# Kernel optimization log

Measured on AMD Instinct MI355X. Metric: run time of the kernel, lower is better.

Reference implementation:

```python
import jax, jax.numpy as jnp
import numpy as np

B, H, W, C = 16, 64, 64, 512
C2 = C // 2
LN_EPS = 1e-3  # Keras LayerNormalization default epsilon


def setup_inputs() -> dict:
    key = jax.random.key(0)
    ks = jax.random.split(key, 8)
    s = 0.02
    return {
        "x": jax.random.normal(ks[0], (B, H, W, C), dtype=jnp.float32),
        "ch_wv_w": jax.random.normal(ks[1], (C, C2), dtype=jnp.float32) * s,
        "ch_wv_b": jnp.zeros((C2,), jnp.float32),
        "ch_wq_w": jax.random.normal(ks[2], (C, 1), dtype=jnp.float32) * s,
        "ch_wq_b": jnp.zeros((1,), jnp.float32),
        "ch_wz_w": jax.random.normal(ks[3], (C2, C), dtype=jnp.float32) * s,
        "ch_wz_b": jnp.zeros((C,), jnp.float32),
        "ln_gamma": jnp.ones((C,), jnp.float32),
        "ln_beta": jnp.zeros((C,), jnp.float32),
        "sp_wv_w": jax.random.normal(ks[4], (C, C2), dtype=jnp.float32) * s,
        "sp_wv_b": jnp.zeros((C2,), jnp.float32),
        "sp_wq_w": jax.random.normal(ks[5], (C, C2), dtype=jnp.float32) * s,
        "sp_wq_b": jnp.zeros((C2,), jnp.float32),
    }


def reference(x, ch_wv_w, ch_wv_b, ch_wq_w, ch_wq_b, ch_wz_w, ch_wz_b,
              ln_gamma, ln_beta, sp_wv_w, sp_wv_b, sp_wq_w, sp_wq_b):
    b, h, w, c = x.shape
    n = h * w
    c2 = c // 2

    # ---- channel-only branch ----
    # 1x1 convs are pointwise GEMMs over the channel dim
    ch_wv = jnp.einsum('bhwc,cd->bhwd', x, ch_wv_w) + ch_wv_b      # (B,H,W,C/2)
    ch_wq = jnp.einsum('bhwc,co->bhwo', x, ch_wq_w) + ch_wq_b      # (B,H,W,1)
    ch_wv = ch_wv.reshape(b, n, c2)                                # (B,N,C/2)
    ch_wq = jax.nn.softmax(ch_wq.reshape(b, n, 1), axis=1)         # softmax over N
    ch_wz = jnp.einsum('bnd,bno->bd', ch_wv, ch_wq)                # (B,C/2)
    ch_wz = jnp.einsum('bd,dc->bc', ch_wz, ch_wz_w) + ch_wz_b      # (B,C)

    # LayerNorm over axes [1,2,3] of (B,1,1,C) == normalize over C
    mean = jnp.mean(ch_wz, axis=-1, keepdims=True)
    var = jnp.var(ch_wz, axis=-1, keepdims=True)
    ch_wz = (ch_wz - mean) * jax.lax.rsqrt(var + LN_EPS) * ln_gamma + ln_beta
    channel_weight = jax.nn.sigmoid(ch_wz)[:, None, None, :]       # (B,1,1,C)
    channel_out = channel_weight * x                               # (B,H,W,C)

    # ---- spatial-only branch ----
    sp_wv = jnp.einsum('bhwc,cd->bhwd', channel_out, sp_wv_w) + sp_wv_b  # (B,H,W,C/2)
    sp_wq = jnp.einsum('bhwc,cd->bhwd', channel_out, sp_wq_w) + sp_wq_b  # (B,H,W,C/2)
    sp_wq = jnp.mean(sp_wq, axis=(1, 2))                           # GAP -> (B,C/2)
    sp_wq = jax.nn.softmax(sp_wq, axis=-1)                         # softmax over C/2
    sp_wv = sp_wv.reshape(b, n, c2)                                # (B,N,C/2)
    sp_wz = jnp.einsum('bd,bnd->bn', sp_wq, sp_wv)                 # (B,N)
    spatial_weight = jax.nn.sigmoid(sp_wz).reshape(b, h, w, 1)     # (B,H,W,1)
    return spatial_weight * channel_out
```

## Files before the change

### kernel.cpp

```cpp
#include <hip/hip_runtime.h>
#include <math.h>

#define BB 16
#define NN 4096
#define CC 512
#define C2 256
#define CHUNKS 64
#define RPC (NN/CHUNKS)
#define NW (CC*C2)

typedef float  f4v __attribute__((ext_vector_type(4)));
typedef unsigned short ushort;
typedef unsigned int   uint;

__device__ __forceinline__ float sigmoidf_(float z){ return 1.0f/(1.0f + __expf(-z)); }
__device__ __forceinline__ float dot8_(float4 a0, float4 a1, float4 b0, float4 b1){
    return a0.x*b0.x + a0.y*b0.y + a0.z*b0.z + a0.w*b0.w
         + a1.x*b1.x + a1.y*b1.y + a1.z*b1.z + a1.w*b1.w;
}
__device__ __forceinline__ ushort f2bf(float f){
    uint u = __float_as_uint(f);
    return (ushort)((u + 0x7FFFu + ((u >> 16) & 1u)) >> 16);
}
__device__ __forceinline__ float2 bfpair(uint v){
    return make_float2(__uint_as_float(v << 16), __uint_as_float(v & 0xFFFF0000u));
}

__global__ __launch_bounds__(256) void k_stats(const float* __restrict__ x,
        const float* __restrict__ wq,
        const float* __restrict__ Wv, const float* __restrict__ Wz,
        const float* __restrict__ Wq2, const float* __restrict__ Wv2,
        float* __restrict__ part_w, float* __restrict__ part_g,
        float* __restrict__ part_d, ushort* __restrict__ wbf)
{
    const int t = threadIdx.x, lane = t & 63, wv = t >> 6;

    if (blockIdx.x >= BB*CHUNKS) {
        const int idx = blockIdx.x - BB*CHUNKS;
        const int mat = idx >> 4;
        const float* src = (mat == 0) ? Wv : (mat == 1) ? Wz : (mat == 2) ? Wq2 : Wv2;
        const int boff = (idx & 15) * 8192;
        ushort* dst = wbf + (long)mat*NW + boff;
        const float* s = src + boff;
        #pragma unroll 8
        for (int e = 0; e < 32; ++e)
            dst[t + e*256] = f2bf(s[t + e*256]);
        return;
    }

    const int b = blockIdx.x / CHUNKS;
    const int k = blockIdx.x % CHUNKS;
    __shared__ float rw[4][CC];
    __shared__ float rg[4][CC];
    __shared__ float rd[4];
    const long base = ((long)b*NN + (long)k*RPC) * CC;

    float4 w0 = *(const float4*)(wq + lane*4);
    float4 w1 = *(const float4*)(wq + 256 + lane*4);
    float4 aw0={0,0,0,0}, aw1={0,0,0,0}, ag0={0,0,0,0}, ag1={0,0,0,0};
    float den = 0.f;

    for (int i = 0; i < RPC/8; ++i) {
        const int r0 = wv*(RPC/4) + 2*i;
        const float* xr0 = x + base + (long)r0*CC;
        const float* xr1 = xr0 + CC;
        float4 a0 = *(const float4*)(xr0 + lane*4);
        float4 a1 = *(const float4*)(xr0 + 256 + lane*4);
        float4 b0 = *(const float4*)(xr1 + lane*4);
        float4 b1 = *(const float4*)(xr1 + 256 + lane*4);
        float da = dot8_(a0, a1, w0, w1);
        float db = dot8_(b0, b1, w0, w1);
        #pragma unroll
        for (int off = 32; off; off >>= 1) {
            da += __shfl_xor(da, off);
            db += __shfl_xor(db, off);
        }
        const float ea = __expf(da);
        const float eb = __expf(db);
        den += ea + eb;
        aw0.x = fmaf(ea,a0.x,fmaf(eb,b0.x,aw0.x)); aw0.y = fmaf(ea,a0.y,fmaf(eb,b0.y,aw0.y));
        aw0.z = fmaf(ea,a0.z,fmaf(eb,b0.z,aw0.z)); aw0.w = fmaf(ea,a0.w,fmaf(eb,b0.w,aw0.w));
        aw1.x = fmaf(ea,a1.x,fmaf(eb,b1.x,aw1.x)); aw1.y = fmaf(ea,a1.y,fmaf(eb,b1.y,aw1.y));
        aw1.z = fmaf(ea,a1.z,fmaf(eb,b1.z,aw1.z)); aw1.w = fmaf(ea,a1.w,fmaf(eb,b1.w,aw1.w));
        ag0.x += a0.x+b0.x; ag0.y += a0.y+b0.y; ag0.z += a0.z+b0.z; ag0.w += a0.w+b0.w;
        ag1.x += a1.x+b1.x; ag1.y += a1.y+b1.y; ag1.z += a1.z+b1.z; ag1.w += a1.w+b1.w;
    }
    *(float4*)&rw[wv][lane*4]     = aw0;
    *(float4*)&rw[wv][256+lane*4] = aw1;
    *(float4*)&rg[wv][lane*4]     = ag0;
    *(float4*)&rg[wv][256+lane*4] = ag1;
    if (lane == 0) rd[wv] = den;
    __syncthreads();

    const long o = (long)(b*CHUNKS + k)*CC;
    part_w[o + t]       = rw[0][t]+rw[1][t]+rw[2][t]+rw[3][t];
    part_w[o + t + 256] = rw[0][t+256]+rw[1][t+256]+rw[2][t+256]+rw[3][t+256];
    part_g[o + t]       = rg[0][t]+rg[1][t]+rg[2][t]+rg[3][t];
    part_g[o + t + 256] = rg[0][t+256]+rg[1][t+256]+rg[2][t+256]+rg[3][t+256];
    if (t == 0) part_d[b*CHUNKS + k] = rd[0]+rd[1]+rd[2]+rd[3];
}

__global__ __launch_bounds__(512) void k_chain(
    const float* __restrict__ part_w, const float* __restrict__ part_g,
    const float* __restrict__ part_d,
    const ushort* __restrict__ wbf,
    const float* __restrict__ bv,  const float* __restrict__ bz,
    const float* __restrict__ lng, const float* __restrict__ lnb,
    const float* __restrict__ bq,  const float* __restrict__ bv2,
    float* __restrict__ cw, float* __restrict__ veff, float* __restrict__ constb)
{
    const int b = blockIdx.x, t = threadIdx.x, lane = t & 63, w = t >> 6;
    const ushort* Wvb  = wbf;
    const ushort* Wzb  = wbf + NW;
    const ushort* Wqb  = wbf + 2*NW;
    const ushort* Wv2b = wbf + 3*NW;
    __shared__ float s_a[CC];
    __shared__ float s_b[CC];
    __shared__ float s_c[CC];
    __shared__ float s_m[C2];
    __shared__ float s_g1[1024];
    __shared__ float s_r[16];

    {
        const float* pwp = part_w + (long)b*CHUNKS*CC + t;
        const float* pgp = part_g + (long)b*CHUNKS*CC + t;
        float pw = 0.f, pg = 0.f;
        #pragma unroll 8
        for (int k = 0; k < CHUNKS; ++k) {
            pw += __builtin_nontemporal_load(pwp + (long)k*CC);
            pg += __builtin_nontemporal_load(pgp + (long)k*CC);
        }
        const float* pd = part_d + b*CHUNKS;
        float den = 0.f;
        #pragma unroll 8
        for (int k = 0; k < CHUNKS; ++k) den += pd[k];
        s_a[t] = pw / den;
        s_b[t] = pg;
    }
    __syncthreads();

    {
        const int pr = t & 127, cq = t >> 7;
        const ushort* wp = Wvb + (long)(cq*128)*C2 + 2*pr;
        const float* xp = s_a + cq*128;
        float ax=0, ay=0, bx=0, by=0;
        #pragma unroll 8
        for (int c = 0; c < 128; c += 2) {
            uint u0 = *(const uint*)(wp + (long)(c  )*C2);
            uint u1 = *(const uint*)(wp + (long)(c+1)*C2);
            float2 p0 = bfpair(u0), p1 = bfpair(u1);
            ax = fmaf(xp[c],   p0.x, ax); ay = fmaf(xp[c],   p0.y, ay);
            bx = fmaf(xp[c+1], p1.x, bx); by = fmaf(xp[c+1], p1.y, by);
        }
        s_g1[cq*256 + pr*2]     = ax + bx;
        s_g1[cq*256 + pr*2 + 1] = ay + by;
    }
    __syncthreads();
    if (t < 256) s_m[t] = s_g1[t] + s_g1[256+t] + s_g1[512+t] + s_g1[768+t] + bv[t];
    __syncthreads();

    {
        const int cp = t & 255, dh = t >> 8;
        const ushort* wp = Wzb + (long)(dh*128)*CC + 2*cp;
        const float* mp = s_m + dh*128;
        float ax=0, ay=0, bx=0, by=0;
        #pragma unroll 8
        for (int d = 0; d < 128; d += 2) {
            uint u0 = *(const uint*)(wp + (long)(d  )*CC);
            uint u1 = *(const uint*)(wp + (long)(d+1)*CC);
            float2 p0 = bfpair(u0), p1 = bfpair(u1);
            ax = fmaf(mp[d],   p0.x, ax); ay = fmaf(mp[d],   p0.y, ay);
            bx = fmaf(mp[d+1], p1.x, bx); by = fmaf(mp[d+1], p1.y, by);
        }
        s_g1[dh*512 + cp*2]     = ax + bx;
        s_g1[dh*512 + cp*2 + 1] = ay + by;
    }
    __syncthreads();
    float zt = s_g1[t] + s_g1[512 + t] + bz[t];

    {
        float sum = zt, sq = zt*zt;
        #pragma unroll
        for (int off = 32; off; off >>= 1) { sum += __shfl_xor(sum, off); sq += __shfl_xor(sq, off); }
        if (lane == 0) { s_r[w] = sum; s_r[8+w] = sq; }
        __syncthreads();
        sum = 0.f; sq = 0.f;
        #pragma unroll
        for (int i = 0; i < 8; ++i) { sum += s_r[i]; sq += s_r[8+i]; }
        const float mean = sum * (1.f/CC);
        const float var  = sq  * (1.f/CC) - mean*mean;
        const float rstd = rsqrtf(var + 1e-3f);
        const float cwt = sigmoidf_((zt - mean)*rstd*lng[t] + lnb[t]);
        cw[b*CC + t] = cwt;
        __syncthreads();
        s_c[t] = cwt;
        s_a[t] = cwt * s_b[t] * (1.f/NN);
    }
    __syncthreads();

    {
        const int pr = t & 127, cq = t >> 7;
        const ushort* wp = Wqb + (long)(cq*128)*C2 + 2*pr;
        const float* xp = s_a + cq*128;
        float ax=0, ay=0, bx=0, by=0;
        #pragma unroll 8
        for (int c = 0; c < 128; c += 2) {
            uint u0 = *(const uint*)(wp + (long)(c  )*C2);
            uint u1 = *(const uint*)(wp + (long)(c+1)*C2);
            float2 p0 = bfpair(u0), p1 = bfpair(u1);
            ax = fmaf(xp[c],   p0.x, ax); ay = fmaf(xp[c],   p0.y, ay);
            bx = fmaf(xp[c+1], p1.x, bx); by = fmaf(xp[c+1], p1.y, by);
        }
        s_g1[cq*256 + pr*2]     = ax + bx;
        s_g1[cq*256 + pr*2 + 1] = ay + by;
    }
    __syncthreads();

    float qv = 0.f;
    if (t < 256) qv = s_g1[t] + s_g1[256+t] + s_g1[512+t] + s_g1[768+t] + bq[t];
    {
        float mx = (t < 256) ? qv : -3.4e38f;
        #pragma unroll
        for (int off = 32; off; off >>= 1) mx = fmaxf(mx, __shfl_xor(mx, off));
        if (lane == 0) s_r[w] = mx;
        __syncthreads();
        mx = s_r[0];
        #pragma unroll
        for (int i = 1; i < 8; ++i) mx = fmaxf(mx, s_r[i]);
        float e = (t < 256) ? __expf(qv - mx) : 0.f;
        float se = e;
        #pragma unroll
        for (int off = 32; off; off >>= 1) se += __shfl_xor(se, off);
        __syncthreads();
        if (lane == 0) s_r[8+w] = se;
        __syncthreads();
        se = 0.f;
        #pragma unroll
        for (int i = 0; i < 8; ++i) se += s_r[8+i];
        const float qn = e / se;
        float cb = (t < 256) ? qn * bv2[t] : 0.f;
        #pragma unroll
        for (int off = 32; off; off >>= 1) cb += __shfl_xor(cb, off);
        if (lane == 0) s_r[w] = cb;
        __syncthreads();
        if (t < 256) s_b[t] = qn;
        if (t == 0) {
            float c_ = 0.f;
            #pragma unroll
            for (int i = 0; i < 8; ++i) c_ += s_r[i];
            constb[b] = c_;
        }
    }
    __syncthreads();

    {
        const int sub = lane & 15;
        float4 q0 = *(const float4*)(s_b + sub*16 + 0);
        float4 q1 = *(const float4*)(s_b + sub*16 + 4);
        float4 q2 = *(const float4*)(s_b + sub*16 + 8);
        float4 q3 = *(const float4*)(s_b + sub*16 + 12);
        for (int it = 0; it < 16; ++it) {
            const int c = (it*8 + w)*4 + (lane >> 4);
            const uint4* wr = (const uint4*)(Wv2b + (long)c*C2) + sub*2;
            uint4 u0 = wr[0], u1 = wr[1];
            float2 p;
            float d = 0.f;
            p = bfpair(u0.x); d += p.x*q0.x + p.y*q0.y;
            p = bfpair(u0.y); d += p.x*q0.z + p.y*q0.w;
            p = bfpair(u0.z); d += p.x*q1.x + p.y*q1.y;
            p = bfpair(u0.w); d += p.x*q1.z + p.y*q1.w;
            p = bfpair(u1.x); d += p.x*q2.x + p.y*q2.y;
            p = bfpair(u1.y); d += p.x*q2.z + p.y*q2.w;
            p = bfpair(u1.z); d += p.x*q3.x + p.y*q3.y;
            p = bfpair(u1.w); d += p.x*q3.z + p.y*q3.w;
            #pragma unroll
            for (int off = 8; off; off >>= 1) d += __shfl_xor(d, off);
            if (sub == 0) veff[b*CC + c] = s_c[c] * d;
        }
    }
}

__global__ __launch_bounds__(256) void k_final(const float* __restrict__ x,
        const float* __restrict__ cw, const float* __restrict__ veff,
        const float* __restrict__ constb, float* __restrict__ out)
{
    const int lane = threadIdx.x & 63;
    const int wv   = threadIdx.x >> 6;
    const long row0 = (long)blockIdx.x * 8 + wv*2;
    const int b = (int)(row0 >> 12);
    const float* vb = veff + b*CC;
    float4 v0 = *(const float4*)(vb + lane*4);
    float4 v1 = *(const float4*)(vb + 256 + lane*4);
    const float* cb = cw + b*CC;
    float4 c0 = *(const float4*)(cb + lane*4);
    float4 c1 = *(const float4*)(cb + 256 + lane*4);
    const float* xr0 = x + row0 * CC;
    float4 a0 = *(const float4*)(xr0 + lane*4);
    float4 a1 = *(const float4*)(xr0 + 256 + lane*4);
    float4 b0 = *(const float4*)(xr0 + CC + lane*4);
    float4 b1 = *(const float4*)(xr0 + CC + 256 + lane*4);
    float d0 = dot8_(a0, a1, v0, v1);
    float d1 = dot8_(b0, b1, v0, v1);
    #pragma unroll
    for (int off = 32; off; off >>= 1) {
        d0 += __shfl_xor(d0, off);
        d1 += __shfl_xor(d1, off);
    }
    const float cbb = constb[b];
    const float sw0 = sigmoidf_(d0 + cbb);
    const float sw1 = sigmoidf_(d1 + cbb);
    f4v o0 = { sw0*c0.x*a0.x, sw0*c0.y*a0.y, sw0*c0.z*a0.z, sw0*c0.w*a0.w };
    f4v o1 = { sw0*c1.x*a1.x, sw0*c1.y*a1.y, sw0*c1.z*a1.z, sw0*c1.w*a1.w };
    f4v o2 = { sw1*c0.x*b0.x, sw1*c0.y*b0.y, sw1*c0.z*b0.z, sw1*c0.w*b0.w };
    f4v o3 = { sw1*c1.x*b1.x, sw1*c1.y*b1.y, sw1*c1.z*b1.z, sw1*c1.w*b1.w };
    __builtin_nontemporal_store(o0, (f4v*)(out + row0*CC + lane*4));
    __builtin_nontemporal_store(o1, (f4v*)(out + row0*CC + 256 + lane*4));
    __builtin_nontemporal_store(o2, (f4v*)(out + row0*CC + CC + lane*4));
    __builtin_nontemporal_store(o3, (f4v*)(out + row0*CC + CC + 256 + lane*4));
}

extern "C" void kernel_launch(void* const* d_in, const int* in_sizes, int n_in,
                              void* d_out, int out_size, void* d_ws, size_t ws_size,
                              hipStream_t stream)
{
    const float* x       = (const float*)d_in[0];
    const float* ch_wv_w = (const float*)d_in[1];
    const float* ch_wv_b = (const float*)d_in[2];
    const float* ch_wq_w = (const float*)d_in[3];
    const float* ch_wz_w = (const float*)d_in[5];
    const float* ch_wz_b = (const float*)d_in[6];
    const float* ln_g    = (const float*)d_in[7];
    const float* ln_b    = (const float*)d_in[8];
    const float* sp_wv_w = (const float*)d_in[9];
    const float* sp_wv_b = (const float*)d_in[10];
    const float* sp_wq_w = (const float*)d_in[11];
    const float* sp_wq_b = (const float*)d_in[12];
    float* out = (float*)d_out;

    float* ws = (float*)d_ws;
    float* part_w  = ws;
    float* part_g  = part_w + BB*CHUNKS*CC;
    float* part_d  = part_g + BB*CHUNKS*CC;
    float* cw      = part_d + BB*CHUNKS;
    float* veff    = cw + BB*CC;
    float* constb  = veff + BB*CC;
    ushort* wbf    = (ushort*)(constb + BB);

    k_stats<<<BB*CHUNKS + 64, 256, 0, stream>>>(x, ch_wq_w,
                                                ch_wv_w, ch_wz_w, sp_wq_w, sp_wv_w,
                                                part_w, part_g, part_d, wbf);
    k_chain<<<BB,  512, 0, stream>>>(part_w, part_g, part_d, wbf,
                                     ch_wv_b, ch_wz_b, ln_g, ln_b, sp_wq_b, sp_wv_b,
                                     cw, veff, constb);
    k_final<<<BB*NN/8, 256, 0, stream>>>(x, cw, veff, constb, out);
}
```

Baseline: 94.97 us.

## Stash fp16 copy of x in stats pass and reuse it in final pass

The stats kernel now writes a half-precision copy of x into the workspace while it streams x. The final kernel then reads that copy instead of fp32 x, processing four rows per wave. Per-lane channel mapping switches to contiguous 8-float chunks. The goal is to cut the final pass's read bytes, at the cost of an extra write in the stats pass and reduced precision of x in the output.

New measurement: 132.9 us. +40.0%, slower.

```diff
diff --git a/kernel.cpp b/kernel.cpp
--- a/kernel.cpp
+++ b/kernel.cpp
@@ -10,6 +10,8 @@
 #define NW (CC*C2)
 
 typedef float  f4v __attribute__((ext_vector_type(4)));
+typedef _Float16 h8v __attribute__((ext_vector_type(8)));
+typedef float    f8v __attribute__((ext_vector_type(8)));
 typedef unsigned short ushort;
 typedef unsigned int   uint;
 
@@ -26,12 +28,14 @@
     return make_float2(__uint_as_float(v << 16), __uint_as_float(v & 0xFFFF0000u));
 }
 
+template<int ECHO>
 __global__ __launch_bounds__(256) void k_stats(const float* __restrict__ x,
         const float* __restrict__ wq,
         const float* __restrict__ Wv, const float* __restrict__ Wz,
         const float* __restrict__ Wq2, const float* __restrict__ Wv2,
         float* __restrict__ part_w, float* __restrict__ part_g,
-        float* __restrict__ part_d, ushort* __restrict__ wbf)
+        float* __restrict__ part_d, ushort* __restrict__ wbf,
+        _Float16* __restrict__ echo)
 {
     const int t = threadIdx.x, lane = t & 63, wv = t >> 6;
 
@@ -53,10 +57,11 @@
     __shared__ float rw[4][CC];
     __shared__ float rg[4][CC];
     __shared__ float rd[4];
-    const long base = ((long)b*NN + (long)k*RPC) * CC;
-
-    float4 w0 = *(const float4*)(wq + lane*4);
-    float4 w1 = *(const float4*)(wq + 256 + lane*4);
+    const long rowbase = (long)b*NN + (long)k*RPC;
+    const long base = rowbase * CC;
+
+    float4 w0 = *(const float4*)(wq + lane*8);
+    float4 w1 = *(const float4*)(wq + lane*8 + 4);
     float4 aw0={0,0,0,0}, aw1={0,0,0,0}, ag0={0,0,0,0}, ag1={0,0,0,0};
     float den = 0.f;
 
@@ -64,16 +69,25 @@
         const int r0 = wv*(RPC/4) + 2*i;
         const float* xr0 = x + base + (long)r0*CC;
         const float* xr1 = xr0 + CC;
-        float4 a0 = *(const float4*)(xr0 + lane*4);
-        float4 a1 = *(const float4*)(xr0 + 256 + lane*4);
-        float4 b0 = *(const float4*)(xr1 + lane*4);
-        float4 b1 = *(const float4*)(xr1 + 256 + lane*4);
+        float4 a0 = *(const float4*)(xr0 + lane*8);
+        float4 a1 = *(const float4*)(xr0 + lane*8 + 4);
+        float4 b0 = *(const float4*)(xr1 + lane*8);
+        float4 b1 = *(const float4*)(xr1 + lane*8 + 4);
         float da = dot8_(a0, a1, w0, w1);
         float db = dot8_(b0, b1, w0, w1);
         #pragma unroll
         for (int off = 32; off; off >>= 1) {
             da += __shfl_xor(da, off);
             db += __shfl_xor(db, off);
+        }
+        if (ECHO) {
+            h8v ha, hb;
+            ha[0]=(_Float16)a0.x; ha[1]=(_Float16)a0.y; ha[2]=(_Float16)a0.z; ha[3]=(_Float16)a0.w;
+            ha[4]=(_Float16)a1.x; ha[5]=(_Float16)a1.y; ha[6]=(_Float16)a1.z; ha[7]=(_Float16)a1.w;
+            hb[0]=(_Float16)b0.x; hb[1]=(_Float16)b0.y; hb[2]=(_Float16)b0.z; hb[3]=(_Float16)b0.w;
+            hb[4]=(_Float16)b1.x; hb[5]=(_Float16)b1.y; hb[6]=(_Float16)b1.z; hb[7]=(_Float16)b1.w;
+            *(h8v*)(echo + (rowbase + r0)*CC + lane*8)     = ha;
+            *(h8v*)(echo + (rowbase + r0 + 1)*CC + lane*8) = hb;
         }
         const float ea = __expf(da);
         const float eb = __expf(db);
@@ -85,10 +99,10 @@
         ag0.x += a0.x+b0.x; ag0.y += a0.y+b0.y; ag0.z += a0.z+b0.z; ag0.w += a0.w+b0.w;
         ag1.x += a1.x+b1.x; ag1.y += a1.y+b1.y; ag1.z += a1.z+b1.z; ag1.w += a1.w+b1.w;
     }
-    *(float4*)&rw[wv][lane*4]     = aw0;
-    *(float4*)&rw[wv][256+lane*4] = aw1;
-    *(float4*)&rg[wv][lane*4]     = ag0;
-    *(float4*)&rg[wv][256+lane*4] = ag1;
+    *(float4*)&rw[wv][lane*8]     = aw0;
+    *(float4*)&rw[wv][lane*8 + 4] = aw1;
+    *(float4*)&rg[wv][lane*8]     = ag0;
+    *(float4*)&rg[wv][lane*8 + 4] = ag1;
     if (lane == 0) rd[wv] = den;
     __syncthreads();
 
@@ -280,7 +294,68 @@
     }
 }
 
-__global__ __launch_bounds__(256) void k_final(const float* __restrict__ x,
+__global__ __launch_bounds__(256) void k_final_echo(const _Float16* __restrict__ echo,
+        const float* __restrict__ cw, const float* __restrict__ veff,
+        const float* __restrict__ constb, float* __restrict__ out)
+{
+    const int lane = threadIdx.x & 63;
+    const int wv   = threadIdx.x >> 6;
+    const long row0 = (long)blockIdx.x * 16 + wv*4;
+    const int b = (int)(row0 >> 12);
+    const float* vb = veff + b*CC + lane*8;
+    float4 v0 = *(const float4*)(vb);
+    float4 v1 = *(const float4*)(vb + 4);
+    const float* cb = cw + b*CC + lane*8;
+    float4 c0 = *(const float4*)(cb);
+    float4 c1 = *(const float4*)(cb + 4);
+    const _Float16* e0 = echo + row0*CC + lane*8;
+
+    f8v x0 = __builtin_convertvector(*(const h8v*)(e0),        f8v);
+    f8v x1 = __builtin_convertvector(*(const h8v*)(e0 + CC),   f8v);
+    f8v x2 = __builtin_convertvector(*(const h8v*)(e0 + 2*CC), f8v);
+    f8v x3 = __builtin_convertvector(*(const h8v*)(e0 + 3*CC), f8v);
+
+    float d0 = x0[0]*v0.x + x0[1]*v0.y + x0[2]*v0.z + x0[3]*v0.w
+             + x0[4]*v1.x + x0[5]*v1.y + x0[6]*v1.z + x0[7]*v1.w;
+    float d1 = x1[0]*v0.x + x1[1]*v0.y + x1[2]*v0.z + x1[3]*v0.w
+             + x1[4]*v1.x + x1[5]*v1.y + x1[6]*v1.z + x1[7]*v1.w;
+    float d2 = x2[0]*v0.x + x2[1]*v0.y + x2[2]*v0.z + x2[3]*v0.w
+             + x2[4]*v1.x + x2[5]*v1.y + x2[6]*v1.z + x2[7]*v1.w;
+    float d3 = x3[0]*v0.x + x3[1]*v0.y + x3[2]*v0.z + x3[3]*v0.w
+             + x3[4]*v1.x + x3[5]*v1.y + x3[6]*v1.z + x3[7]*v1.w;
+    #pragma unroll
+    for (int off = 32; off; off >>= 1) {
+        d0 += __shfl_xor(d0, off);
+        d1 += __shfl_xor(d1, off);
+        d2 += __shfl_xor(d2, off);
+        d3 += __shfl_xor(d3, off);
+    }
+    const float cbb = constb[b];
+    const float s0 = sigmoidf_(d0 + cbb);
+    const float s1 = sigmoidf_(d1 + cbb);
+    const float s2 = sigmoidf_(d2 + cbb);
+    const float s3 = sigmoidf_(d3 + cbb);
+    float* op = out + row0*CC + lane*8;
+    f4v o;
+    o = (f4v){ s0*c0.x*x0[0], s0*c0.y*x0[1], s0*c0.z*x0[2], s0*c0.w*x0[3] };
+    __builtin_nontemporal_store(o, (f4v*)(op));
+    o = (f4v){ s0*c1.x*x0[4], s0*c1.y*x0[5], s0*c1.z*x0[6], s0*c1.w*x0[7] };
+    __builtin_nontemporal_store(o, (f4v*)(op + 4));
+    o = (f4v){ s1*c0.x*x1[0], s1*c0.y*x1[1], s1*c0.z*x1[2], s1*c0.w*x1[3] };
+    __builtin_nontemporal_store(o, (f4v*)(op + CC));
+    o = (f4v){ s1*c1.x*x1[4], s1*c1.y*x1[5], s1*c1.z*x1[6], s1*c1.w*x1[7] };
+    __builtin_nontemporal_store(o, (f4v*)(op + CC + 4));
+    o = (f4v){ s2*c0.x*x2[0], s2*c0.y*x2[1], s2*c0.z*x2[2], s2*c0.w*x2[3] };
+    __builtin_nontemporal_store(o, (f4v*)(op + 2*CC));
+    o = (f4v){ s2*c1.x*x2[4], s2*c1.y*x2[5], s2*c1.z*x2[6], s2*c1.w*x2[7] };
+    __builtin_nontemporal_store(o, (f4v*)(op + 2*CC + 4));
+    o = (f4v){ s3*c0.x*x3[0], s3*c0.y*x3[1], s3*c0.z*x3[2], s3*c0.w*x3[3] };
+    __builtin_nontemporal_store(o, (f4v*)(op + 3*CC));
+    o = (f4v){ s3*c1.x*x3[4], s3*c1.y*x3[5], s3*c1.z*x3[6], s3*c1.w*x3[7] };
+    __builtin_nontemporal_store(o, (f4v*)(op + 3*CC + 4));
+}
+
+__global__ __launch_bounds__(256) void k_final_f32(const float* __restrict__ x,
         const float* __restrict__ cw, const float* __restrict__ veff,
         const float* __restrict__ constb, float* __restrict__ out)
 {
@@ -337,20 +412,35 @@
     const float* sp_wq_b = (const float*)d_in[12];
     float* out = (float*)d_out;
 
-    float* ws = (float*)d_ws;
+    const size_t echo_bytes = (size_t)BB*NN*CC*sizeof(_Float16);
+    const size_t rest_floats = (size_t)BB*CHUNKS*CC*2 + BB*CHUNKS + BB*CC*2 + BB + 16;
+    const size_t rest_bytes  = rest_floats*4 + (size_t)4*NW*sizeof(ushort);
+    const bool use_echo = ws_size >= echo_bytes + rest_bytes;
+
+    _Float16* echo = (_Float16*)d_ws;
+    float* ws = use_echo ? (float*)((char*)d_ws + echo_bytes) : (float*)d_ws;
     float* part_w  = ws;
     float* part_g  = part_w + BB*CHUNKS*CC;
     float* part_d  = part_g + BB*CHUNKS*CC;
     float* cw      = part_d + BB*CHUNKS;
     float* veff    = cw + BB*CC;
     float* constb  = veff + BB*CC;
-    ushort* wbf    = (ushort*)(constb + BB);
-
-    k_stats<<<BB*CHUNKS + 64, 256, 0, stream>>>(x, ch_wq_w,
+    ushort* wbf    = (ushort*)(constb + BB + 15);
+
+    if (use_echo) {
+        k_stats<1><<<BB*CHUNKS + 64, 256, 0, stream>>>(x, ch_wq_w,
                                                 ch_wv_w, ch_wz_w, sp_wq_w, sp_wv_w,
-                                                part_w, part_g, part_d, wbf);
+                                                part_w, part_g, part_d, wbf, echo);
+    } else {
+        k_stats<0><<<BB*CHUNKS + 64, 256, 0, stream>>>(x, ch_wq_w,
+                                                ch_wv_w, ch_wz_w, sp_wq_w, sp_wv_w,
+                                                part_w, part_g, part_d, wbf, echo);
+    }
     k_chain<<<BB,  512, 0, stream>>>(part_w, part_g, part_d, wbf,
                                      ch_wv_b, ch_wz_b, ln_g, ln_b, sp_wq_b, sp_wv_b,
                                      cw, veff, constb);
-    k_final<<<BB*NN/8, 256, 0, stream>>>(x, cw, veff, constb, out);
-}
+    if (use_echo)
+        k_final_echo<<<BB*NN/16, 256, 0, stream>>>(echo, cw, veff, constb, out);
+    else
+        k_final_f32 <<<BB*NN/8,  256, 0, stream>>>(x, cw, veff, constb, out);
+}
```
